# Performance work log

Measured on AMD Instinct MI355X. Metric: run time of the kernel, lower is better.

## Reference

```python
import jax, jax.numpy as jnp
import numpy as np
from jax import lax

DIM = 256; HEADS = 16; DHEAD = 16; H = 12; W = 26
DS = 4; KOFF = 6; OSCALE = 4.0
SCALE = DHEAD ** -0.5
EPS = 1e-5


def _create_grid(hh, ww, dtype):
    # channel0 = x (width index), channel1 = y (height index); matches torch meshgrid(arange(w), arange(h), indexing='xy')
    gy, gx = jnp.meshgrid(jnp.arange(hh, dtype=dtype), jnp.arange(ww, dtype=dtype), indexing='ij')
    return jnp.stack([gx, gy], axis=0)  # (2, hh, ww)


def _grid_sample_bilinear(img, grid):
    # F.grid_sample, mode='bilinear', padding_mode='zeros', align_corners=False
    # img (B,C,Hi,Wi); grid (B,Ho,Wo,2), grid[...,0]=x-norm, grid[...,1]=y-norm in [-1,1]
    B, C, Hi, Wi = img.shape
    x = ((grid[..., 0] + 1.0) * Wi - 1.0) / 2.0
    y = ((grid[..., 1] + 1.0) * Hi - 1.0) / 2.0
    x0 = jnp.floor(x); y0 = jnp.floor(y)

    def gather(xi, yi):
        valid = ((xi >= 0) & (xi < Wi) & (yi >= 0) & (yi < Hi)).astype(img.dtype)
        xc = jnp.clip(xi, 0, Wi - 1).astype(jnp.int32)
        yc = jnp.clip(yi, 0, Hi - 1).astype(jnp.int32)
        v = jax.vmap(lambda im, yy, xx: im[:, yy, xx])(img, yc, xc)  # (B,C,Ho,Wo)
        return v * valid[:, None]

    wx1 = (x - x0)[:, None]; wx0 = 1.0 - wx1
    wy1 = (y - y0)[:, None]; wy0 = 1.0 - wy1
    return (gather(x0, y0) * wy0 * wx0 + gather(x0 + 1.0, y0) * wy0 * wx1
            + gather(x0, y0 + 1.0) * wy1 * wx0 + gather(x0 + 1.0, y0 + 1.0) * wy1 * wx1)


def _forward(x, q, w_off_dw, b_off_dw, w_off_pw, wk, wv, w_out, b_out,
             cpb_w1, cpb_b1, cpb_w2, cpb_b2, cpb_w3, cpb_b3,
             conv1d_w, conv1d_b, ln_g, ln_b):
    b = x.shape[0]
    # faithful to torch: q.repeat(1,1,h*w).view(bs,1,dim,h,w).squeeze(1) == tile then reshape
    q_map = jnp.tile(q[:, 0, :], (1, H * W)).reshape(b, DIM, H, W)

    # to_offsets: depthwise Conv2d(k=6,s=4,p=1) -> GELU -> 1x1 conv (no bias) -> tanh -> *offset_scale
    t = lax.conv_general_dilated(q_map, w_off_dw, window_strides=(DS, DS),
                                 padding=[(1, 1), (1, 1)], feature_group_count=DIM,
                                 dimension_numbers=('NCHW', 'OIHW', 'NCHW'))
    t = jax.nn.gelu(t + b_off_dw[None, :, None, None], approximate=False)
    off = jnp.tanh(jnp.einsum('oc,bchw->bohw', w_off_pw, t)) * OSCALE  # (b,2,Hk,Wk)
    Hk, Wk = off.shape[-2], off.shape[-1]  # 3, 6

    gkv = _create_grid(Hk, Wk, x.dtype)
    vg0 = gkv[0] + off[:, 0]
    vg1 = gkv[1] + off[:, 1]
    # faithful repo normalize_grid: channel0 / (h-1), channel1 / (w-1)
    n0 = 2.0 * vg0 / max(Hk - 1, 1) - 1.0
    n1 = 2.0 * vg1 / max(Wk - 1, 1) - 1.0
    vgrid_scaled = jnp.stack([n0, n1], axis=-1)  # (b, Hk, Wk, 2)

    kv = _grid_sample_bilinear(x, vgrid_scaled)  # (b, DIM, Hk, Wk)
    k = jnp.einsum('oc,bchw->bohw', wk, kv)
    v = jnp.einsum('oc,bchw->bohw', wv, kv)

    qh = (q_map * SCALE).reshape(b, HEADS, DHEAD, H * W).transpose(0, 1, 3, 2)  # (b,h,i,d)
    kh = k.reshape(b, HEADS, DHEAD, Hk * Wk).transpose(0, 1, 3, 2)              # (b,h,j,d)
    vh = v.reshape(b, HEADS, DHEAD, Hk * Wk).transpose(0, 1, 3, 2)
    sim = jnp.einsum('bhid,bhjd->bhij', qh, kh)  # (b,16,312,18)

    # CPB relative position bias
    gq = _create_grid(H, W, x.dtype)
    gq0 = 2.0 * gq[0] / max(H - 1, 1) - 1.0
    gq1 = 2.0 * gq[1] / max(W - 1, 1) - 1.0
    grid_q = jnp.stack([gq0, gq1], axis=-1).reshape(1, H * W, 2)
    grid_kv = vgrid_scaled.reshape(b, Hk * Wk, 2)
    pos = grid_q[:, :, None, :] - grid_kv[:, None, :, :]       # (b,i,j,2)
    bias = jnp.sign(pos) * jnp.log(jnp.abs(pos) + 1.0)
    bias = jax.nn.relu(bias @ cpb_w1.T + cpb_b1)
    bias = jax.nn.relu(bias @ cpb_w2.T + cpb_b2)
    bias = bias @ cpb_w3.T + cpb_b3                             # (b,i,j,heads)
    sim = sim + bias.transpose(0, 3, 1, 2)

    attn = jax.nn.softmax(sim, axis=-1)  # dropout(0.1) identity in eval
    out = jnp.einsum('bhij,bhjd->bhid', attn, vh)               # (b,h,i,d)
    out = out.transpose(0, 1, 3, 2).reshape(b, DIM, H, W)        # 'b h (x y) d -> b (h d) x y'
    out = jnp.einsum('oc,bchw->bohw', w_out, out) + b_out[None, :, None, None]

    # SpatialCrossAttention tail: view -> permute -> Conv1d(312,1,1) -> residual -> LayerNorm
    tokens = out.reshape(b, DIM, H * W).transpose(0, 2, 1)       # (b,312,256)
    pooled = jnp.einsum('t,btc->bc', conv1d_w, tokens)[:, None, :] + conv1d_b[None, :, None]
    y = pooled + q
    mu = y.mean(-1, keepdims=True)
    var = y.var(-1, keepdims=True)
    return (y - mu) / jnp.sqrt(var + EPS) * ln_g + ln_b          # (b,1,256)


def setup_inputs() -> dict:
    key = jax.random.key(0)
    ks = jax.random.split(key, 16)
    rn = lambda i, shape, s=0.02: jax.random.normal(ks[i], shape, dtype=jnp.float32) * s
    B = 256
    return {
        'x': jax.random.normal(ks[0], (B, DIM, H, W), dtype=jnp.float32),
        'q': jax.random.normal(ks[1], (B, 1, DIM), dtype=jnp.float32),
        'w_off_dw': rn(2, (DIM, 1, KOFF, KOFF), 0.05),
        'b_off_dw': jnp.zeros((DIM,), jnp.float32),
        'w_off_pw': rn(3, (2, DIM), 0.05),
        'wk': rn(4, (DIM, DIM)),
        'wv': rn(5, (DIM, DIM)),
        'w_out': rn(6, (DIM, DIM)),
        'b_out': jnp.zeros((DIM,), jnp.float32),
        'cpb_w1': rn(7, (64, 2), 0.1),
        'cpb_b1': jnp.zeros((64,), jnp.float32),
        'cpb_w2': rn(8, (64, 64), 0.1),
        'cpb_b2': jnp.zeros((64,), jnp.float32),
        'cpb_w3': rn(9, (HEADS, 64), 0.1),
        'cpb_b3': jnp.zeros((HEADS,), jnp.float32),
        'conv1d_w': rn(10, (H * W,), 0.05),
        'conv1d_b': jnp.zeros((1,), jnp.float32),
        'ln_g': jnp.ones((DIM,), jnp.float32),
        'ln_b': jnp.zeros((DIM,), jnp.float32),
    }


def reference(x, q, w_off_dw, b_off_dw, w_off_pw, wk, wv, w_out, b_out,
              cpb_w1, cpb_b1, cpb_w2, cpb_b2, cpb_w3, cpb_b3,
              conv1d_w, conv1d_b, ln_g, ln_b):
    return _forward(x, q, w_off_dw, b_off_dw, w_off_pw, wk, wv, w_out, b_out,
                    cpb_w1, cpb_b1, cpb_w2, cpb_b2, cpb_w3, cpb_b3,
                    conv1d_w, conv1d_b, ln_g, ln_b)
```

## Files before the change

kernel.cpp:

```cpp
#include <hip/hip_runtime.h>
#include <math.h>


typedef __attribute__((ext_vector_type(8))) short short8;
typedef __attribute__((ext_vector_type(4))) float floatx4;

union U16 { uint4 u; short8 s; };

#define MFMA(A, B, C) __builtin_amdgcn_mfma_f32_16x16x32_bf16((A), (B), (C), 0, 0, 0)

__device__ __forceinline__ unsigned int f2bf(float f) {
    unsigned int u = __float_as_uint(f);
    u += 0x7fffu + ((u >> 16) & 1u);
    return u >> 16;
}
__device__ __forceinline__ unsigned int pk2(float a, float b) {
    return f2bf(a) | (f2bf(b) << 16);
}
__device__ __forceinline__ float bf2f(unsigned short v) {
    return __uint_as_float((unsigned int)v << 16);
}
__device__ __forceinline__ uint4 pack8(float4 a, float4 b) {
    uint4 r;
    r.x = pk2(a.x, a.y); r.y = pk2(a.z, a.w);
    r.z = pk2(b.x, b.y); r.w = pk2(b.z, b.w);
    return r;
}

__global__ __launch_bounds__(512, 2) void k_all(
    const float* __restrict__ x, const float* __restrict__ q,
    const float* __restrict__ w_dw, const float* __restrict__ b_dw,
    const float* __restrict__ w_pw,
    const float* __restrict__ wk, const float* __restrict__ wv,
    const float* __restrict__ w_out, const float* __restrict__ b_out,
    const float* __restrict__ cw1, const float* __restrict__ cb1,
    const float* __restrict__ cw2, const float* __restrict__ cb2,
    const float* __restrict__ cw3, const float* __restrict__ cb3,
    const float* __restrict__ conv_w, const float* __restrict__ conv_b,
    const float* __restrict__ ln_g, const float* __restrict__ ln_b,
    float* __restrict__ out)
{
    const int b = blockIdx.x, tid = threadIdx.x;
    const int w = tid >> 6, lane = tid & 63;
    const int n = lane & 15, qd = lane >> 4;

    __shared__ float qf_s[256];
    __shared__ unsigned short q_sb[256];
    __shared__ unsigned short v_sb[5120];
    __shared__ float F0[468], F1[216];
    __shared__ unsigned int lutxy[312];
    __shared__ float off_s[36], n0_s[18], n1_s[18];
    __shared__ float sx0[18], sy0[18], swx[18], swy[18];
    __shared__ float b2_s[64], b3_s[16];
    __shared__ float wA_s[288];
    __shared__ __align__(16) float m_s[256];
    __shared__ float pooled_s[256], redb[24];
    __shared__ __align__(16) unsigned char UB[39168];
    float* S_ = (float*)UB;
    unsigned short* kvT = (unsigned short*)UB;
    float* qsw = (float*)UB;
    float* t_s = (float*)(UB + 16512);
    unsigned short* k_sb = (unsigned short*)(UB + 16512);
    float* wred = (float*)UB;

    uint4 W2f[4][2], W3f[2];
    {
        const float4* cw2_4 = (const float4*)cw2;
        #pragma unroll
        for (int mtl = 0; mtl < 4; ++mtl)
            #pragma unroll
            for (int ks = 0; ks < 2; ++ks) {
                const int base = (mtl * 16 + n) * 16 + ks * 8 + qd * 2;
                W2f[mtl][ks] = pack8(cw2_4[base], cw2_4[base + 1]);
            }
        const float4* cw3_4 = (const float4*)cw3;
        #pragma unroll
        for (int ks = 0; ks < 2; ++ks) {
            const int base = n * 16 + ks * 8 + qd * 2;
            W3f[ks] = pack8(cw3_4[base], cw3_4[base + 1]);
        }
    }
    float W1a[16], W1b[16], B1r[16];
    #pragma unroll
    for (int kk = 0; kk < 16; ++kk) {
        const int kid = (kk < 8) ? (qd * 8 + kk) : (32 + qd * 8 + kk - 8);
        W1a[kk] = cw1[kid * 2]; W1b[kk] = cw1[kid * 2 + 1]; B1r[kk] = cb1[kid];
    }

    if (tid < 256) {
        const float qv = q[b * 256 + tid];
        qf_s[tid] = qv;
        q_sb[tid] = (unsigned short)f2bf(qv * 0.25f);
    }
    for (int u = tid; u < 4128; u += 512) {
        const int r = u / 258, i = u - r * 258;
        qsw[u] = (i < 256) ? q[b * 256 + i] : 0.f;
    }
    if (tid < 312) {
        const int iy = tid / 26;
        lutxy[tid] = (unsigned int)(tid - iy * 26) | ((unsigned int)iy << 16);
    }
    if (tid < 64) b2_s[tid] = cb2[tid];
    if (tid < 16) b3_s[tid] = cb3[tid];
    __syncthreads();

    {
        const int c = tid & 255, g = tid >> 8;
        float wreg[36];
        const float4* wdw4 = (const float4*)w_dw;
        #pragma unroll
        for (int i = 0; i < 9; ++i) {
            const float4 t4 = wdw4[c * 9 + i];
            wreg[i * 4 + 0] = t4.x; wreg[i * 4 + 1] = t4.y;
            wreg[i * 4 + 2] = t4.z; wreg[i * 4 + 3] = t4.w;
        }
        float acc[9];
        const float bv = b_dw[c];
        #pragma unroll
        for (int a = 0; a < 9; ++a) acc[a] = bv;
        const int cb = (c * 56) & 255;
        const int cp = (c & 15) * 258;
        for (int jh = 0; jh < 3; ++jh) {
            for (int kh = 0; kh < 6; ++kh) {
                const int ih = jh * 4 - 1 + kh;
                if (ih < 0 || ih >= 12) continue;
                const int rb = ih * 26;
                #pragma unroll
                for (int jwl = 0; jwl < 3; ++jwl) {
                    const int jw = g * 3 + jwl;
                    #pragma unroll
                    for (int kw = 0; kw < 6; ++kw) {
                        const int iw = jw * 4 - 1 + kw;
                        if (iw < 0 || iw >= 26) continue;
                        acc[jh * 3 + jwl] += wreg[kh * 6 + kw] * qsw[cp + ((cb + rb + iw) & 255)];
                    }
                }
            }
        }
        #pragma unroll
        for (int a = 0; a < 9; ++a) {
            const int jh = a / 3, jwl = a - jh * 3;
            const int p = jh * 6 + g * 3 + jwl;
            const float v = acc[a];
            t_s[p * 256 + c] = 0.5f * v * (1.0f + erff(v * 0.70710678118654752f));
        }
    }
    __syncthreads();

    for (int oi = w; oi < 36; oi += 8) {
        const int o = oi / 18, p = oi - o * 18;
        float s = 0.f;
        for (int c = lane; c < 256; c += 64) s += w_pw[o * 256 + c] * t_s[p * 256 + c];
        for (int d = 32; d > 0; d >>= 1) s += __shfl_down(s, d, 64);
        if (lane == 0) off_s[oi] = 4.0f * tanhf(s);
    }
    __syncthreads();

    if (tid < 18) {
        const int j = tid, jh = j / 6, jw = j - jh * 6;
        const float vg0 = (float)jw + off_s[j];
        const float vg1 = (float)jh + off_s[18 + j];
        const float n0 = 2.0f * vg0 / 2.0f - 1.0f;
        const float n1 = 2.0f * vg1 / 5.0f - 1.0f;
        n0_s[j] = n0; n1_s[j] = n1;
        const float xp = ((n0 + 1.0f) * 26.0f - 1.0f) * 0.5f;
        const float yp = ((n1 + 1.0f) * 12.0f - 1.0f) * 0.5f;
        const float x0 = floorf(xp), y0 = floorf(yp);
        sx0[j] = x0; sy0[j] = y0; swx[j] = xp - x0; swy[j] = yp - y0;
    }
    __syncthreads();

    {
        const int c = tid & 255, g = tid >> 8;
        const float* xb = x + ((size_t)b * 256 + c) * 312;
        for (int jj = 0; jj < 9; ++jj) {
            const int j = g * 9 + jj;
            const int x0 = (int)sx0[j], y0 = (int)sy0[j];
            const int x1 = x0 + 1, y1 = y0 + 1;
            const float wx1 = swx[j], wy1 = swy[j];
            const float wx0 = 1.f - wx1, wy0 = 1.f - wy1;
            const bool xv0 = (x0 >= 0) & (x0 < 26), xv1 = (x1 >= 0) & (x1 < 26);
            const bool yv0 = (y0 >= 0) & (y0 < 12), yv1 = (y1 >= 0) & (y1 < 12);
            const float v00 = (xv0 & yv0) ? xb[y0 * 26 + x0] : 0.f;
            const float v01 = (xv1 & yv0) ? xb[y0 * 26 + x1] : 0.f;
            const float v10 = (xv0 & yv1) ? xb[y1 * 26 + x0] : 0.f;
            const float v11 = (xv1 & yv1) ? xb[y1 * 26 + x1] : 0.f;
            const float val = wy0 * (wx0 * v00 + wx1 * v01) + wy1 * (wx0 * v10 + wx1 * v11);
            kvT[j * 264 + c] = (unsigned short)f2bf(val);
        }
    }
    for (int u = tid; u < 684; u += 512) {
        if (u < 468) {
            const int ixv = u / 18, j = u - ixv * 18;
            const float p0 = (float)ixv * (2.0f / 11.0f) - 1.0f - n0_s[j];
            F0[u] = copysignf(__logf(1.0f + fabsf(p0)), p0);
        } else {
            const int u2 = u - 468;
            const int iyv = u2 / 18, j = u2 - iyv * 18;
            const float p1 = (float)iyv * (2.0f / 25.0f) - 1.0f - n1_s[j];
            F1[u2] = copysignf(__logf(1.0f + fabsf(p1)), p1);
        }
    }
    __syncthreads();

    {
        const int m2 = w & 1, mtb = w >> 1;
        const float4* wm4 = (const float4*)(m2 ? wv : wk);
        floatx4 pa[4][2];
        #pragma unroll
        for (int a = 0; a < 4; ++a) {
            pa[a][0] = (floatx4){0.f, 0.f, 0.f, 0.f};
            pa[a][1] = (floatx4){0.f, 0.f, 0.f, 0.f};
        }
        #pragma unroll 2
        for (int ks = 0; ks < 8; ++ks) {
            U16 b0, b1;
            b0.u = *(const uint4*)(kvT + n * 264 + ks * 32 + qd * 8);
            b1.u = make_uint4(0u, 0u, 0u, 0u);
            if (n < 2) b1.u = *(const uint4*)(kvT + (16 + n) * 264 + ks * 32 + qd * 8);
            #pragma unroll
            for (int mtl = 0; mtl < 4; ++mtl) {
                const int mt = mtb + mtl * 4;
                const int fb = (mt * 16 + n) * 16 + ks * 2 + qd * 2 * 1;
                const int f4i = (mt * 16 + n) * 64 + ks * 8 + qd * 2;
                U16 A; A.u = pack8(wm4[f4i], wm4[f4i + 1]);
                (void)fb;
                pa[mtl][0] = MFMA(A.s, b0.s, pa[mtl][0]);
                pa[mtl][1] = MFMA(A.s, b1.s, pa[mtl][1]);
            }
        }
        unsigned short* dst = m2 ? v_sb : k_sb;
        #pragma unroll
        for (int mtl = 0; mtl < 4; ++mtl) {
            const int mt = mtb + mtl * 4;
            #pragma unroll
            for (int r = 0; r < 4; ++r) {
                const int o = mt * 16 + qd * 4 + r;
                dst[o * 20 + n] = (unsigned short)f2bf(pa[mtl][0][r]);
                if (n < 2) dst[o * 20 + 16 + n] = (unsigned short)f2bf(pa[mtl][1][r]);
            }
        }
    }
    __syncthreads();

    uint4 BkU[2][2];
    #pragma unroll
    for (int hh = 0; hh < 2; ++hh)
        #pragma unroll
        for (int jt = 0; jt < 2; ++jt) {
            unsigned int u0 = 0, u1 = 0, u2 = 0, u3 = 0;
            if (qd < 2 && (jt == 0 || n < 2)) {
                const int h = w * 2 + hh;
                const int j = jt * 16 + n;
                const int cb0 = (h * 16 + qd * 8) * 20 + j;
                u0 = (unsigned)k_sb[cb0] | ((unsigned)k_sb[cb0 + 20] << 16);
                u1 = (unsigned)k_sb[cb0 + 40] | ((unsigned)k_sb[cb0 + 60] << 16);
                u2 = (unsigned)k_sb[cb0 + 80] | ((unsigned)k_sb[cb0 + 100] << 16);
                u3 = (unsigned)k_sb[cb0 + 120] | ((unsigned)k_sb[cb0 + 140] << 16);
            }
            BkU[hh][jt] = make_uint4(u0, u1, u2, u3);
        }
    __syncthreads();

    float wAcc[18];
    #pragma unroll
    for (int j = 0; j < 18; ++j) wAcc[j] = 0.f;

    const int srcA = n + ((lane & 16) << 1);
    const int srcB = srcA + 16;
    const bool hi2 = (qd & 2) != 0;

    for (int ch = 0; ch < 10; ++ch) {
        const int ibase = ch * 32;
        const int CI = (ch == 9) ? 24 : 32;

        #pragma unroll
        for (int hh = 0; hh < 2; ++hh) {
            const int h = w * 2 + hh;
            const int base = h * 16 + qd * 8;
            #pragma unroll
            for (int ig = 0; ig < 2; ++ig) {
                unsigned int a0 = 0, a1 = 0, a2 = 0, a3u = 0;
                if (qd < 2) {
                    const int ii = ibase + ig * 16 + n;
                    a0 = (unsigned)q_sb[((base + 0) * 56 + ii) & 255] |
                         ((unsigned)q_sb[((base + 1) * 56 + ii) & 255] << 16);
                    a1 = (unsigned)q_sb[((base + 2) * 56 + ii) & 255] |
                         ((unsigned)q_sb[((base + 3) * 56 + ii) & 255] << 16);
                    a2 = (unsigned)q_sb[((base + 4) * 56 + ii) & 255] |
                         ((unsigned)q_sb[((base + 5) * 56 + ii) & 255] << 16);
                    a3u = (unsigned)q_sb[((base + 6) * 56 + ii) & 255] |
                          ((unsigned)q_sb[((base + 7) * 56 + ii) & 255] << 16);
                }
                U16 Af; Af.u = make_uint4(a0, a1, a2, a3u);
                #pragma unroll
                for (int jt = 0; jt < 2; ++jt) {
                    U16 Bf; Bf.u = BkU[hh][jt];
                    floatx4 D = {0.f, 0.f, 0.f, 0.f};
                    D = MFMA(Af.s, Bf.s, D);
                    const int j = jt * 16 + n;
                    if (j < 18) {
                        #pragma unroll
                        for (int r = 0; r < 4; ++r)
                            S_[((ig * 16 + qd * 4 + r) * 18 + j) * 17 + h] = D[r];
                    }
                }
            }
        }
        __syncthreads();

        {
            auto mlp2 = [&](int tA, int tB, bool doB) {
                const int tv2[2] = {tA, tB};
                U16 ub0[2], ub1[2];
                #pragma unroll
                for (int u2 = 0; u2 < 2; ++u2) {
                    const int t = tv2[u2];
                    const int ig = (t >= 18) ? 1 : 0;
                    const int j = t - ig * 18;
                    const int i0 = ibase + ig * 16 + n;
                    const unsigned int lv = lutxy[(i0 < 312) ? i0 : 311];
                    const int ix = (int)(lv & 0xffffu), iy = (int)(lv >> 16);
                    const float f0 = F0[ix * 18 + j];
                    const float f1 = F1[iy * 18 + j];
                    unsigned int uu[8];
                    #pragma unroll
                    for (int kp = 0; kp < 8; ++kp) {
                        const float ha = fmaxf(fmaf(W1a[2*kp],   f0, fmaf(W1b[2*kp],   f1, B1r[2*kp])),   0.f);
                        const float hb = fmaxf(fmaf(W1a[2*kp+1], f0, fmaf(W1b[2*kp+1], f1, B1r[2*kp+1])), 0.f);
                        uu[kp] = pk2(ha, hb);
                    }
                    ub0[u2].u = make_uint4(uu[0], uu[1], uu[2], uu[3]);
                    ub1[u2].u = make_uint4(uu[4], uu[5], uu[6], uu[7]);
                }
                unsigned int Pa[2][4], Pb[2][4];
                #pragma unroll
                for (int u2 = 0; u2 < 2; ++u2) {
                    #pragma unroll
                    for (int mtl = 0; mtl < 4; ++mtl) {
                        U16 A0, A1; A0.u = W2f[mtl][0]; A1.u = W2f[mtl][1];
                        floatx4 acc = {0.f, 0.f, 0.f, 0.f};
                        acc = MFMA(A0.s, ub0[u2].s, acc);
                        acc = MFMA(A1.s, ub1[u2].s, acc);
                        const float e0 = fmaxf(acc[0] + b2_s[mtl*16 + qd*4 + 0], 0.f);
                        const float e1 = fmaxf(acc[1] + b2_s[mtl*16 + qd*4 + 1], 0.f);
                        const float e2 = fmaxf(acc[2] + b2_s[mtl*16 + qd*4 + 2], 0.f);
                        const float e3 = fmaxf(acc[3] + b2_s[mtl*16 + qd*4 + 3], 0.f);
                        Pa[u2][mtl] = pk2(e0, e1);
                        Pb[u2][mtl] = pk2(e2, e3);
                    }
                }
                #pragma unroll
                for (int u2 = 0; u2 < 2; ++u2) {
                    unsigned int qa[4], qb[4], ra[4], rb[4];
                    #pragma unroll
                    for (int m = 0; m < 4; ++m) {
                        qa[m] = __shfl(Pa[u2][m], srcA, 64);
                        qb[m] = __shfl(Pb[u2][m], srcA, 64);
                        ra[m] = __shfl(Pa[u2][m], srcB, 64);
                        rb[m] = __shfl(Pb[u2][m], srcB, 64);
                    }
                    U16 uc0, uc1;
                    uc0.u = make_uint4(hi2 ? qa[1] : qa[0], hi2 ? qb[1] : qb[0],
                                       hi2 ? ra[1] : ra[0], hi2 ? rb[1] : rb[0]);
                    uc1.u = make_uint4(hi2 ? qa[3] : qa[2], hi2 ? qb[3] : qb[2],
                                       hi2 ? ra[3] : ra[2], hi2 ? rb[3] : rb[2]);
                    U16 A0, A1; A0.u = W3f[0]; A1.u = W3f[1];
                    floatx4 a3 = {0.f, 0.f, 0.f, 0.f};
                    a3 = MFMA(A0.s, uc0.s, a3);
                    a3 = MFMA(A1.s, uc1.s, a3);
                    if (u2 == 0 || doB) {
                        const int t = tv2[u2];
                        const int ig = (t >= 18) ? 1 : 0;
                        const int j = t - ig * 18;
                        float* sp = S_ + ((ig * 16 + n) * 18 + j) * 17 + qd * 4;
                        #pragma unroll
                        for (int r = 0; r < 4; ++r) sp[r] = a3[r] + b3_s[qd * 4 + r] + sp[r];
                    }
                }
            };
            mlp2(w, w + 8, true);
            mlp2(w + 16, w + 24, true);
            if (w < 4) mlp2(32 + w, 32 + w, false);
        }
        __syncthreads();

        {
            const int il = tid >> 4, h = tid & 15;
            if (il < CI) {
                float lv[18];
                #pragma unroll
                for (int j = 0; j < 18; ++j) lv[j] = S_[(il * 18 + j) * 17 + h];
                float m = lv[0];
                #pragma unroll
                for (int j = 1; j < 18; ++j) m = fmaxf(m, lv[j]);
                float s = 0.f;
                #pragma unroll
                for (int j = 0; j < 18; ++j) { lv[j] = __expf(lv[j] - m); s += lv[j]; }
                const float wgt = conv_w[ibase + il] / s;
                #pragma unroll
                for (int j = 0; j < 18; ++j) wAcc[j] = fmaf(wgt, lv[j], wAcc[j]);
            }
        }
        __syncthreads();
    }

    #pragma unroll
    for (int j = 0; j < 18; ++j) wred[tid * 18 + j] = wAcc[j];
    {
        float v = 0.f;
        for (int u = tid; u < 312; u += 512) v += conv_w[u];
        for (int d = 32; d > 0; d >>= 1) v += __shfl_down(v, d, 64);
        if (lane == 0) redb[w] = v;
    }
    __syncthreads();
    for (int u = tid; u < 288; u += 512) {
        const int h = u / 18, j = u - h * 18;
        float s = 0.f;
        #pragma unroll
        for (int sl = 0; sl < 32; ++sl) s += wred[(sl * 16 + h) * 18 + j];
        wA_s[u] = s;
    }
    __syncthreads();

    if (tid < 256) {
        const int hb = (tid >> 4) * 18;
        float acc = 0.f;
        #pragma unroll
        for (int j = 0; j < 18; ++j) acc += wA_s[hb + j] * bf2f(v_sb[tid * 20 + j]);
        m_s[tid] = acc;
    }
    __syncthreads();

    float Ssum = 0.f;
    #pragma unroll
    for (int i = 0; i < 8; ++i) Ssum += redb[i];

    {
        const float4 mm = *(const float4*)(m_s + lane * 4);
        for (int ol = 0; ol < 32; ++ol) {
            const int o = w * 32 + ol;
            const float4 wq = *(const float4*)(w_out + o * 256 + lane * 4);
            float d = wq.x * mm.x + wq.y * mm.y + wq.z * mm.z + wq.w * mm.w;
            for (int dd = 32; dd > 0; dd >>= 1) d += __shfl_down(d, dd, 64);
            if (lane == 0) pooled_s[o] = d;
        }
    }
    __syncthreads();

    if (tid < 256) {
        const float y = pooled_s[tid] + b_out[tid] * Ssum + conv_b[0] + qf_s[tid];
        float s1 = y, s2 = y * y;
        for (int d = 32; d > 0; d >>= 1) { s1 += __shfl_down(s1, d, 64); s2 += __shfl_down(s2, d, 64); }
        if (lane == 0) { redb[16 + w] = s1; redb[20 + w] = s2; }
    }
    __syncthreads();
    if (tid < 256) {
        const float y = pooled_s[tid] + b_out[tid] * Ssum + conv_b[0] + qf_s[tid];
        const float S1 = redb[16] + redb[17] + redb[18] + redb[19];
        const float S2 = redb[20] + redb[21] + redb[22] + redb[23];
        const float mu = S1 * (1.0f / 256.0f);
        const float var = S2 * (1.0f / 256.0f) - mu * mu;
        out[b * 256 + tid] = (y - mu) * rsqrtf(var + 1e-5f) * ln_g[tid] + ln_b[tid];
    }
}

extern "C" void kernel_launch(void* const* d_in, const int* in_sizes, int n_in,
                              void* d_out, int out_size, void* d_ws, size_t ws_size,
                              hipStream_t stream) {
    const float* x       = (const float*)d_in[0];
    const float* q       = (const float*)d_in[1];
    const float* w_dw    = (const float*)d_in[2];
    const float* b_dwp   = (const float*)d_in[3];
    const float* w_pw    = (const float*)d_in[4];
    const float* wk      = (const float*)d_in[5];
    const float* wv      = (const float*)d_in[6];
    const float* w_out   = (const float*)d_in[7];
    const float* b_out   = (const float*)d_in[8];
    const float* cw1     = (const float*)d_in[9];
    const float* cb1     = (const float*)d_in[10];
    const float* cw2     = (const float*)d_in[11];
    const float* cb2     = (const float*)d_in[12];
    const float* cw3     = (const float*)d_in[13];
    const float* cb3     = (const float*)d_in[14];
    const float* conv_w  = (const float*)d_in[15];
    const float* conv_b  = (const float*)d_in[16];
    const float* ln_g    = (const float*)d_in[17];
    const float* ln_b    = (const float*)d_in[18];
    float* out = (float*)d_out;

    k_all<<<256, 512, 0, stream>>>(x, q, w_dw, b_dwp, w_pw, wk, wv, w_out, b_out,
                                   cw1, cb1, cw2, cb2, cw3, cb3,
                                   conv_w, conv_b, ln_g, ln_b, out);
}
```

Measured before the change: 268.9 us.

## Double-buffer score tiles, overlap softmax with next chunk, stage MLP hidden in LDS

Score storage becomes two ping-pong buffers, so the softmax and conv-weighted accumulation for chunk ch-1 runs alongside the QK MFMA writes for chunk ch. This removes one block-wide barrier per chunk. The cross-lane shuffles that rearranged the CPB MLP hidden layer into MFMA B-fragments are replaced by an LDS store and vector reload through a new per-wave region. Float-to-bf16 packing now uses the HIP bf16 pair intrinsic. The shared buffer grows from about 39 KB to about 113 KB, which likely stops two 512-thread blocks from fitting on one CU as the launch bounds request.

```diff
diff --git a/kernel.cpp b/kernel.cpp
--- a/kernel.cpp
+++ b/kernel.cpp
@@ -1,4 +1,5 @@
 #include <hip/hip_runtime.h>
+#include <hip/hip_bf16.h>
 #include <math.h>
 
 
@@ -15,7 +16,9 @@
     return u >> 16;
 }
 __device__ __forceinline__ unsigned int pk2(float a, float b) {
-    return f2bf(a) | (f2bf(b) << 16);
+    __hip_bfloat162 h = __float22bfloat162_rn(make_float2(a, b));
+    union { __hip_bfloat162 h; unsigned int u; } cv; cv.h = h;
+    return cv.u;
 }
 __device__ __forceinline__ float bf2f(unsigned short v) {
     return __uint_as_float((unsigned int)v << 16);
@@ -55,12 +58,13 @@
     __shared__ float wA_s[288];
     __shared__ __align__(16) float m_s[256];
     __shared__ float pooled_s[256], redb[24];
-    __shared__ __align__(16) unsigned char UB[39168];
-    float* S_ = (float*)UB;
+    __shared__ __align__(16) unsigned char UB[113152];
+    float* Sbuf = (float*)UB;
     unsigned short* kvT = (unsigned short*)UB;
     float* qsw = (float*)UB;
     float* t_s = (float*)(UB + 16512);
     unsigned short* k_sb = (unsigned short*)(UB + 16512);
+    unsigned int* h2w = (unsigned int*)(UB + 78336);
     float* wred = (float*)UB;
 
     uint4 W2f[4][2], W3f[2];
@@ -221,10 +225,8 @@
             #pragma unroll
             for (int mtl = 0; mtl < 4; ++mtl) {
                 const int mt = mtb + mtl * 4;
-                const int fb = (mt * 16 + n) * 16 + ks * 2 + qd * 2 * 1;
                 const int f4i = (mt * 16 + n) * 64 + ks * 8 + qd * 2;
                 U16 A; A.u = pack8(wm4[f4i], wm4[f4i + 1]);
-                (void)fb;
                 pa[mtl][0] = MFMA(A.s, b0.s, pa[mtl][0]);
                 pa[mtl][1] = MFMA(A.s, b1.s, pa[mtl][1]);
             }
@@ -266,13 +268,30 @@
     #pragma unroll
     for (int j = 0; j < 18; ++j) wAcc[j] = 0.f;
 
-    const int srcA = n + ((lane & 16) << 1);
-    const int srcB = srcA + 16;
-    const bool hi2 = (qd & 2) != 0;
+    auto soft_acc = [&](int chp, const float* Sp) {
+        const int il = tid >> 4, h = tid & 15;
+        const int CIp = (chp == 9) ? 24 : 32;
+        if (il < CIp) {
+            const float cwv = conv_w[chp * 32 + il];
+            float lv[18];
+            #pragma unroll
+            for (int j = 0; j < 18; ++j) lv[j] = Sp[(il * 18 + j) * 17 + h];
+            float m = lv[0];
+            #pragma unroll
+            for (int j = 1; j < 18; ++j) m = fmaxf(m, lv[j]);
+            float s = 0.f;
+            #pragma unroll
+            for (int j = 0; j < 18; ++j) { lv[j] = __expf(lv[j] - m); s += lv[j]; }
+            const float wgt = cwv / s;
+            #pragma unroll
+            for (int j = 0; j < 18; ++j) wAcc[j] = fmaf(wgt, lv[j], wAcc[j]);
+        }
+    };
 
     for (int ch = 0; ch < 10; ++ch) {
+        float* Sc = Sbuf + (ch & 1) * 9792;
+        const float* Sp = Sbuf + ((ch & 1) ^ 1) * 9792;
         const int ibase = ch * 32;
-        const int CI = (ch == 9) ? 24 : 32;
 
         #pragma unroll
         for (int hh = 0; hh < 2; ++hh) {
@@ -302,15 +321,16 @@
                     if (j < 18) {
                         #pragma unroll
                         for (int r = 0; r < 4; ++r)
-                            S_[((ig * 16 + qd * 4 + r) * 18 + j) * 17 + h] = D[r];
+                            Sc[((ig * 16 + qd * 4 + r) * 18 + j) * 17 + h] = D[r];
                     }
                 }
             }
         }
+        if (ch > 0) soft_acc(ch - 1, Sp);
         __syncthreads();
 
         {
-            auto mlp2 = [&](int tA, int tB, bool doB) {
+            auto mlp2 = [&](int tA, int tB, bool two) {
                 const int tv2[2] = {tA, tB};
                 U16 ub0[2], ub1[2];
                 #pragma unroll
@@ -319,8 +339,8 @@
                     const int ig = (t >= 18) ? 1 : 0;
                     const int j = t - ig * 18;
                     const int i0 = ibase + ig * 16 + n;
-                    const unsigned int lv = lutxy[(i0 < 312) ? i0 : 311];
-                    const int ix = (int)(lv & 0xffffu), iy = (int)(lv >> 16);
+                    const unsigned int lv2 = lutxy[(i0 < 312) ? i0 : 311];
+                    const int ix = (int)(lv2 & 0xffffu), iy = (int)(lv2 >> 16);
                     const float f0 = F0[ix * 18 + j];
                     const float f1 = F1[iy * 18 + j];
                     unsigned int uu[8];
@@ -333,9 +353,10 @@
                     ub0[u2].u = make_uint4(uu[0], uu[1], uu[2], uu[3]);
                     ub1[u2].u = make_uint4(uu[4], uu[5], uu[6], uu[7]);
                 }
-                unsigned int Pa[2][4], Pb[2][4];
                 #pragma unroll
                 for (int u2 = 0; u2 < 2; ++u2) {
+                    if (u2 == 1 && !two) break;
+                    unsigned int* hw = h2w + ((w << 1) | u2) * 544 + n * 34;
                     #pragma unroll
                     for (int mtl = 0; mtl < 4; ++mtl) {
                         U16 A0, A1; A0.u = W2f[mtl][0]; A1.u = W2f[mtl][1];
@@ -346,37 +367,27 @@
                         const float e1 = fmaxf(acc[1] + b2_s[mtl*16 + qd*4 + 1], 0.f);
                         const float e2 = fmaxf(acc[2] + b2_s[mtl*16 + qd*4 + 2], 0.f);
                         const float e3 = fmaxf(acc[3] + b2_s[mtl*16 + qd*4 + 3], 0.f);
-                        Pa[u2][mtl] = pk2(e0, e1);
-                        Pb[u2][mtl] = pk2(e2, e3);
+                        hw[mtl * 8 + qd * 2]     = pk2(e0, e1);
+                        hw[mtl * 8 + qd * 2 + 1] = pk2(e2, e3);
                     }
                 }
                 #pragma unroll
                 for (int u2 = 0; u2 < 2; ++u2) {
-                    unsigned int qa[4], qb[4], ra[4], rb[4];
-                    #pragma unroll
-                    for (int m = 0; m < 4; ++m) {
-                        qa[m] = __shfl(Pa[u2][m], srcA, 64);
-                        qb[m] = __shfl(Pb[u2][m], srcA, 64);
-                        ra[m] = __shfl(Pa[u2][m], srcB, 64);
-                        rb[m] = __shfl(Pb[u2][m], srcB, 64);
-                    }
+                    if (u2 == 1 && !two) break;
+                    const unsigned int* hwr = h2w + ((w << 1) | u2) * 544;
                     U16 uc0, uc1;
-                    uc0.u = make_uint4(hi2 ? qa[1] : qa[0], hi2 ? qb[1] : qb[0],
-                                       hi2 ? ra[1] : ra[0], hi2 ? rb[1] : rb[0]);
-                    uc1.u = make_uint4(hi2 ? qa[3] : qa[2], hi2 ? qb[3] : qb[2],
-                                       hi2 ? ra[3] : ra[2], hi2 ? rb[3] : rb[2]);
+                    uc0.u = *(const uint4*)(hwr + n * 34 + qd * 4);
+                    uc1.u = *(const uint4*)(hwr + n * 34 + 16 + qd * 4);
                     U16 A0, A1; A0.u = W3f[0]; A1.u = W3f[1];
                     floatx4 a3 = {0.f, 0.f, 0.f, 0.f};
                     a3 = MFMA(A0.s, uc0.s, a3);
                     a3 = MFMA(A1.s, uc1.s, a3);
-                    if (u2 == 0 || doB) {
-                        const int t = tv2[u2];
-                        const int ig = (t >= 18) ? 1 : 0;
-                        const int j = t - ig * 18;
-                        float* sp = S_ + ((ig * 16 + n) * 18 + j) * 17 + qd * 4;
-                        #pragma unroll
-                        for (int r = 0; r < 4; ++r) sp[r] = a3[r] + b3_s[qd * 4 + r] + sp[r];
-                    }
+                    const int t = tv2[u2];
+                    const int ig = (t >= 18) ? 1 : 0;
+                    const int j = t - ig * 18;
+                    float* sp = Sc + ((ig * 16 + n) * 18 + j) * 17 + qd * 4;
+                    #pragma unroll
+                    for (int r = 0; r < 4; ++r) sp[r] = a3[r] + b3_s[qd * 4 + r] + sp[r];
                 }
             };
             mlp2(w, w + 8, true);
@@ -384,26 +395,8 @@
             if (w < 4) mlp2(32 + w, 32 + w, false);
         }
         __syncthreads();
-
-        {
-            const int il = tid >> 4, h = tid & 15;
-            if (il < CI) {
-                float lv[18];
-                #pragma unroll
-                for (int j = 0; j < 18; ++j) lv[j] = S_[(il * 18 + j) * 17 + h];
-                float m = lv[0];
-                #pragma unroll
-                for (int j = 1; j < 18; ++j) m = fmaxf(m, lv[j]);
-                float s = 0.f;
-                #pragma unroll
-                for (int j = 0; j < 18; ++j) { lv[j] = __expf(lv[j] - m); s += lv[j]; }
-                const float wgt = conv_w[ibase + il] / s;
-                #pragma unroll
-                for (int j = 0; j < 18; ++j) wAcc[j] = fmaf(wgt, lv[j], wAcc[j]);
-            }
-        }
-        __syncthreads();
-    }
+    }
+    soft_acc(9, Sbuf + 9792);
 
     #pragma unroll
     for (int j = 0; j < 18; ++j) wred[tid * 18 + j] = wAcc[j];
```

Result: no change. 265.4 us (-1.3%).
